# Performance work log

Measured on AMD Instinct MI355X. Metric: run time of the kernel, lower is better.

## Reference

```python
import jax, jax.numpy as jnp
import numpy as np

D_MODEL = 1024
N_HEAD = 16
HEAD_DIM = D_MODEL // N_HEAD  # 64
D_FF = 4096
BATCH = 4
SEQ = 2048
EPS = 1e-5
ROPE_BASE = 10000.0


def _xavier(key, shape):
    fan_in, fan_out = shape[1], shape[0]
    limit = np.sqrt(6.0 / (fan_in + fan_out))
    return jax.random.uniform(key, shape, jnp.float32, -limit, limit)


def setup_inputs() -> dict:
    key = jax.random.key(0)
    ks = jax.random.split(key, 8)
    return {
        "src": jax.random.normal(ks[0], (BATCH, SEQ, D_MODEL), jnp.float32),
        "Wqkv": _xavier(ks[1], (3 * D_MODEL, D_MODEL)),   # torch Linear weight layout [out,in]
        "Wout": _xavier(ks[2], (D_MODEL, D_MODEL)),
        "g1": jnp.ones((D_MODEL,), jnp.float32),           # RMSNorm weights
        "g2": jnp.ones((D_MODEL,), jnp.float32),
        "W1": _xavier(ks[3], (D_FF, D_MODEL)),              # GeGLU w1
        "W2": _xavier(ks[4], (D_MODEL, D_FF)),              # GeGLU w2
        "W3": _xavier(ks[5], (D_FF, D_MODEL)),              # GeGLU w3
    }


def _rmsnorm(x, g, eps=EPS):
    return x * jax.lax.rsqrt(jnp.mean(x * x, axis=-1, keepdims=True) + eps) * g


def _rope(x):
    # x: [B, H, S, head_dim], interleaved even/odd rotation (matches torch stack+flatten)
    seq = x.shape[-2]
    inv_freq = 1.0 / (ROPE_BASE ** (jnp.arange(0, HEAD_DIM, 2, dtype=jnp.float32) / HEAD_DIM))
    t = jnp.arange(seq, dtype=jnp.float32)
    freqs = t[:, None] * inv_freq[None, :]          # [S, head_dim/2]
    cos, sin = jnp.cos(freqs), jnp.sin(freqs)
    x = x.astype(jnp.float32)
    x_even = x[..., 0::2]
    x_odd = x[..., 1::2]
    rot_even = x_even * cos - x_odd * sin
    rot_odd = x_odd * cos + x_even * sin
    return jnp.stack([rot_even, rot_odd], axis=-1).reshape(x.shape)


def reference(src, Wqkv, Wout, g1, g2, W1, W2, W3):
    B, S, _ = src.shape
    # --- attention block (pre-norm) ---
    xn = _rmsnorm(src, g1)
    qkv = xn @ Wqkv.T                                        # [B,S,3*D]
    qkv = qkv.reshape(B, S, 3, N_HEAD, HEAD_DIM).transpose(2, 0, 3, 1, 4)  # [3,B,H,S,hd]
    q, k, v = qkv[0], qkv[1], qkv[2]
    q = _rope(q)
    k = _rope(k)
    scale = 1.0 / jnp.sqrt(jnp.float32(HEAD_DIM))
    scores = jnp.einsum("bhqd,bhkd->bhqk", q, k) * scale
    probs = jax.nn.softmax(scores, axis=-1)
    attn = jnp.einsum("bhqk,bhkd->bhqd", probs, v)           # [B,H,S,hd]
    attn = attn.transpose(0, 2, 1, 3).reshape(B, S, D_MODEL)
    x = src + attn @ Wout.T
    # --- GeGLU FFN block (pre-norm) ---
    xn2 = _rmsnorm(x, g2)
    ff = (jax.nn.gelu(xn2 @ W1.T, approximate=False) * (xn2 @ W3.T)) @ W2.T
    return x + ff
```

## Files before the change

kernel.cpp:

```cpp
#include <hip/hip_runtime.h>

#define DEVI __device__ __forceinline__

typedef __attribute__((ext_vector_type(8))) short s8v;
typedef __attribute__((ext_vector_type(4))) float f4v;

DEVI unsigned short f2bf(float f) {
  unsigned int u = __float_as_uint(f);
  return (unsigned short)((u + 0x7FFFu + ((u >> 16) & 1u)) >> 16);
}
DEVI float bf2f(unsigned short h) { return __uint_as_float(((unsigned int)h) << 16); }

DEVI f4v mfma16(s8v a, s8v b, f4v c) {
  asm("v_mfma_f32_16x16x32_bf16 %0, %1, %2, %0" : "+v"(c) : "v"(a), "v"(b));
  return c;
}

DEVI float fexp2(float x) {
  float r;
  asm("v_exp_f32 %0, %1" : "=v"(r) : "v"(x));
  return r;
}

DEVI unsigned int cvtpk_bf16(float lo, float hi) {
  unsigned int r;
  asm("v_cvt_pk_bf16_f32 %0, %1, %2" : "=v"(r) : "v"(lo), "v"(hi));
  return r;
}

DEVI float gelu_t(float x) {
  const float t = x * x;
  const float a = __builtin_fmaf(t, -0.10295555f, -2.30225854f);
  return x / (1.0f + fexp2(x * a));
}

DEVI void gload_lds16(const void* g, void* l) {
  __builtin_amdgcn_global_load_lds(
      (__attribute__((address_space(1))) void*)g,
      (__attribute__((address_space(3))) void*)l, 16, 0, 0);
}

DEVI void barrier_raw() {
  asm volatile("" ::: "memory");
  __builtin_amdgcn_s_barrier();
  asm volatile("" ::: "memory");
}

DEVI void map_block(int bid, int nbx, int gw, int& by, int& bx) {
  const int xcd = bid & 7;
  const int local = bid >> 3;
  const int grp = gw * 8;
  const int q = local / grp;
  const int rem = local - q * grp;
  by = xcd * 8 + (rem & 7);
  bx = q * gw + (rem >> 3);
}

__global__ __launch_bounds__(256)
void cvt_all_k(const float* __restrict__ Wqkv, const float* __restrict__ Wout,
               const float* __restrict__ W2, const float* __restrict__ W1,
               const float* __restrict__ W3,
               unsigned short* __restrict__ wQKV, unsigned short* __restrict__ wOut,
               unsigned short* __restrict__ wW2, unsigned short* __restrict__ wI) {
  const int i = blockIdx.x * 256 + threadIdx.x;
  const float4* src;
  ushort4* dst;
  if (i < 786432) {
    src = (const float4*)Wqkv + i;
    dst = (ushort4*)wQKV + i;
  } else if (i < 1048576) {
    const int j = i - 786432;
    src = (const float4*)Wout + j;
    dst = (ushort4*)wOut + j;
  } else if (i < 2097152) {
    const int j = i - 1048576;
    src = (const float4*)W2 + j;
    dst = (ushort4*)wW2 + j;
  } else {
    const int j = i - 2097152;
    const int g = j >> 8;
    const int c4 = j & 255;
    const int srow = ((g >> 7) << 6) + (g & 63);
    const float* s = ((g >> 6) & 1) ? W3 : W1;
    src = (const float4*)(s + (size_t)srow * 1024) + c4;
    dst = (ushort4*)(wI + (size_t)g * 1024) + c4;
  }
  const float4 v = *src;
  ushort4 ov;
  ov.x = f2bf(v.x); ov.y = f2bf(v.y); ov.z = f2bf(v.z); ov.w = f2bf(v.w);
  *dst = ov;
}

__global__ __launch_bounds__(256)
void rmsnorm_k(const float* __restrict__ x, const float* __restrict__ g,
               unsigned short* __restrict__ o) {
  const int row = blockIdx.x;
  const int tid = threadIdx.x;
  const float4 v = ((const float4*)(x + (size_t)row * 1024))[tid];
  float ss = v.x * v.x + v.y * v.y + v.z * v.z + v.w * v.w;
#pragma unroll
  for (int off = 32; off > 0; off >>= 1) ss += __shfl_down(ss, off);
  __shared__ float wsum[4];
  if ((tid & 63) == 0) wsum[tid >> 6] = ss;
  __syncthreads();
  const float tot = wsum[0] + wsum[1] + wsum[2] + wsum[3];
  const float sc = rsqrtf(tot * (1.0f / 1024.0f) + 1e-5f);
  const float4 gv = ((const float4*)g)[tid];
  ushort4 ov;
  ov.x = f2bf(v.x * sc * gv.x);
  ov.y = f2bf(v.y * sc * gv.y);
  ov.z = f2bf(v.z * sc * gv.z);
  ov.w = f2bf(v.w * sc * gv.w);
  ((ushort4*)(o + (size_t)row * 1024))[tid] = ov;
}

__global__ __launch_bounds__(256)
void rmsnorm_b(const unsigned short* __restrict__ x, const float* __restrict__ g,
               unsigned short* __restrict__ o) {
  const int row = blockIdx.x;
  const int tid = threadIdx.x;
  const ushort4 hv = ((const ushort4*)(x + (size_t)row * 1024))[tid];
  float v0 = bf2f(hv.x), v1 = bf2f(hv.y), v2 = bf2f(hv.z), v3 = bf2f(hv.w);
  float ss = v0 * v0 + v1 * v1 + v2 * v2 + v3 * v3;
#pragma unroll
  for (int off = 32; off > 0; off >>= 1) ss += __shfl_down(ss, off);
  __shared__ float wsum[4];
  if ((tid & 63) == 0) wsum[tid >> 6] = ss;
  __syncthreads();
  const float tot = wsum[0] + wsum[1] + wsum[2] + wsum[3];
  const float sc = rsqrtf(tot * (1.0f / 1024.0f) + 1e-5f);
  const float4 gv = ((const float4*)g)[tid];
  ushort4 ov;
  ov.x = f2bf(v0 * sc * gv.x);
  ov.y = f2bf(v1 * sc * gv.y);
  ov.z = f2bf(v2 * sc * gv.z);
  ov.w = f2bf(v3 * sc * gv.w);
  ((ushort4*)(o + (size_t)row * 1024))[tid] = ov;
}

__global__ __launch_bounds__(256)
void rope_table_k(float* __restrict__ cosT, float* __restrict__ sinT) {
  const int idx = blockIdx.x * 256 + threadIdx.x;
  const int s = idx >> 5, p = idx & 31;
  const float inv = powf(10000.0f, -(float)(2 * p) * (1.0f / 64.0f));
  const float a = (float)s * inv;
  cosT[idx] = cosf(a);
  sinT[idx] = sinf(a);
}

__global__ __launch_bounds__(256)
void vtrans_k(const unsigned short* __restrict__ v, unsigned short* __restrict__ vT) {
  __shared__ unsigned short t[64][72];
  const int bh = blockIdx.y;
  const int s0 = blockIdx.x * 64;
  const int tid = threadIdx.x;
  const int r = tid >> 3;
  const int c8 = (tid & 7) * 8;
  const unsigned short* src = v + ((size_t)bh * 2048 + s0) * 64;
#pragma unroll
  for (int it = 0; it < 2; ++it) {
    const int row = it * 32 + r;
    s8v d = *(const s8v*)(src + row * 64 + c8);
    *(s8v*)(&t[row][c8]) = d;
  }
  __syncthreads();
  unsigned short* dst = vT + (size_t)bh * 64 * 2048 + s0;
#pragma unroll
  for (int it = 0; it < 2; ++it) {
    const int d = it * 32 + r;
    s8v o;
#pragma unroll
    for (int m = 0; m < 8; ++m) o[m] = (short)t[c8 + m][d];
    *(s8v*)(dst + (size_t)d * 2048 + c8) = o;
  }
}

template <int EPI>
__global__ __launch_bounds__(256)
void gemm_bt(const unsigned short* __restrict__ A,
             const unsigned short* __restrict__ Bt,
             const int K, const int N, const int nbx, const int gw,
             unsigned short* Cb, float* Cf, const float* Xadd,
             unsigned short* __restrict__ Qp, unsigned short* __restrict__ Kp,
             unsigned short* __restrict__ Vp,
             const float* __restrict__ cosT, const float* __restrict__ sinT) {
  __shared__ __align__(16) unsigned char sA[128 * 128];
  __shared__ __align__(16) unsigned char sB[128 * 128];
  const int tid = threadIdx.x;
  const int lane = tid & 63;
  const int wave = tid >> 6;
  const int wr = (wave >> 1) * 64, wc = (wave & 1) * 64;
  int by, bx;
  map_block(blockIdx.x, nbx, gw, by, bx);
  const int row0 = by * 128;
  const int col0 = bx * 128;

  int ldsOff[4], gOffA[4], gOffB[4];
#pragma unroll
  for (int it = 0; it < 4; ++it) {
    const int p = it * 4096 + tid * 16;
    const int row = p >> 7;
    const int inner = (p & 127) ^ ((row & 7) << 4);
    ldsOff[it] = p;
    gOffA[it] = (row0 + row) * K + (inner >> 1);
    gOffB[it] = (col0 + row) * K + (inner >> 1);
  }

  f4v acc[4][4];
  const f4v fzero = {0.f, 0.f, 0.f, 0.f};
#pragma unroll
  for (int i = 0; i < 4; ++i)
#pragma unroll
    for (int j = 0; j < 4; ++j) acc[i][j] = fzero;

  const int cbase = (lane >> 4) * 16;
  const int rlane = lane & 15;

  for (int kt = 0; kt < K; kt += 64) {
    __syncthreads();
#pragma unroll
    for (int it = 0; it < 4; ++it) {
      gload_lds16(A + gOffA[it] + kt, sA + ldsOff[it]);
      gload_lds16(Bt + gOffB[it] + kt, sB + ldsOff[it]);
    }
    asm volatile("s_waitcnt vmcnt(0)" ::: "memory");
    __syncthreads();

#pragma unroll
    for (int ks = 0; ks < 2; ++ks) {
      const int cb = ks * 64 + cbase;
      s8v af[4], bfv[4];
#pragma unroll
      for (int i = 0; i < 4; ++i) {
        const int r = wr + i * 16 + rlane;
        af[i] = *(const s8v*)(sA + r * 128 + (cb ^ ((r & 7) << 4)));
      }
#pragma unroll
      for (int j = 0; j < 4; ++j) {
        const int r = wc + j * 16 + rlane;
        bfv[j] = *(const s8v*)(sB + r * 128 + (cb ^ ((r & 7) << 4)));
      }
#pragma unroll
      for (int i = 0; i < 4; ++i)
#pragma unroll
        for (int j = 0; j < 4; ++j) acc[i][j] = mfma16(af[i], bfv[j], acc[i][j]);
    }
  }

  const int rquad = (lane >> 4) * 4;

  if constexpr (EPI == 4) {
    __syncthreads();
    float* xbuf = (wave & 2) ? (float*)sB : (float*)sA;
    if (wave & 1) {
#pragma unroll
      for (int i = 0; i < 2; ++i)
#pragma unroll
        for (int j = 0; j < 4; ++j)
#pragma unroll
          for (int r = 0; r < 4; ++r)
            xbuf[((i * 16 + rquad + r) << 6) + j * 16 + rlane] = acc[i][j][r];
    } else {
#pragma unroll
      for (int i = 0; i < 2; ++i)
#pragma unroll
        for (int j = 0; j < 4; ++j)
#pragma unroll
          for (int r = 0; r < 4; ++r)
            xbuf[2048 + ((i * 16 + rquad + r) << 6) + j * 16 + rlane] = acc[2 + i][j][r];
    }
    __syncthreads();
    if (!(wave & 1)) {
#pragma unroll
      for (int i = 0; i < 2; ++i)
#pragma unroll
        for (int j = 0; j < 4; ++j)
#pragma unroll
          for (int r = 0; r < 4; ++r) {
            const int t = i * 16 + rquad + r;
            const float h1v = acc[i][j][r];
            const float h3v = xbuf[(t << 6) + j * 16 + rlane];
            Cb[(size_t)(row0 + wr + t) * N + (size_t)bx * 64 + j * 16 + rlane] =
                f2bf(gelu_t(h1v) * h3v);
          }
    } else {
#pragma unroll
      for (int i = 0; i < 2; ++i)
#pragma unroll
        for (int j = 0; j < 4; ++j)
#pragma unroll
          for (int r = 0; r < 4; ++r) {
            const int t = i * 16 + rquad + r;
            const float h1v = xbuf[2048 + (t << 6) + j * 16 + rlane];
            const float h3v = acc[2 + i][j][r];
            Cb[(size_t)(row0 + wr + 32 + t) * N + (size_t)bx * 64 + j * 16 + rlane] =
                f2bf(gelu_t(h1v) * h3v);
          }
    }
    return;
  }

#pragma unroll
  for (int i = 0; i < 4; ++i) {
#pragma unroll
    for (int j = 0; j < 4; ++j) {
#pragma unroll
      for (int r = 0; r < 4; ++r) {
        const int row = row0 + wr + i * 16 + rquad + r;
        const int col = col0 + wc + j * 16 + rlane;
        const float v = acc[i][j][r];
        if constexpr (EPI == 1) {
          const float partner = __shfl_xor(v, 1);
          const int which = col >> 10;
          const int rem = col & 1023;
          const int s = row & 2047;
          const int p = (rem & 63) >> 1;
          const float c = cosT[(s << 5) + p];
          const float sn = sinT[(s << 5) + p];
          const float sg = (rem & 1) ? sn : -sn;
          const float roped = __builtin_fmaf(partner, sg, v * c);
          const size_t idx =
              (((size_t)(row >> 11) * 16 + (rem >> 6)) * 2048 + (row & 2047)) * 64 + (rem & 63);
          if (which == 0) Qp[idx] = f2bf(roped * (0.125f * 1.44269504089f));
          else if (which == 1) Kp[idx] = f2bf(roped);
          else Vp[idx] = f2bf(v);
        } else if constexpr (EPI == 5) {
          const size_t idx = (size_t)row * N + col;
          Cb[idx] = f2bf(Xadd[idx] + v);
        } else {
          const size_t idx = (size_t)row * N + col;
          Cf[idx] = bf2f(Qp[idx]) + v;
        }
      }
    }
  }
}

__global__ __launch_bounds__(256)
void attn_k(const unsigned short* __restrict__ Qg,
            const unsigned short* __restrict__ Kg,
            const unsigned short* __restrict__ VTg,
            unsigned short* __restrict__ Og) {
  __shared__ __align__(16) unsigned char sK[2][8192];
  __shared__ __align__(16) unsigned char sV[2][8192];

  const int tid = threadIdx.x, lane = tid & 63, wave = tid >> 6;
  int id = blockIdx.x;
  id = (id & 7) * 128 + (id >> 3);
  const int qt = id & 15, h = (id >> 4) & 15, b = id >> 8;
  const size_t bh = (size_t)b * 16 + h;
  const unsigned short* qb = Qg + (bh * 2048 + (size_t)qt * 128 + wave * 32) * 64;
  const unsigned short* kbp = Kg + bh * 2048 * 64;
  const unsigned short* vb = VTg + bh * 64 * 2048;

  const int g = lane >> 4;
  const int rl = lane & 15;
  const int cbase = g * 16;

  s8v qf[2][2];
#pragma unroll
  for (int qs = 0; qs < 2; ++qs) {
    const unsigned short* qrow = qb + (size_t)(qs * 16 + rl) * 64 + g * 8;
    qf[qs][0] = *(const s8v*)(qrow);
    qf[qs][1] = *(const s8v*)(qrow + 32);
  }

  const f4v fzero = {0.f, 0.f, 0.f, 0.f};
  f4v of[2][4];
#pragma unroll
  for (int qs = 0; qs < 2; ++qs)
#pragma unroll
    for (int jd = 0; jd < 4; ++jd) of[qs][jd] = fzero;
  float l[2] = {0.f, 0.f};

  int ldsOff[2], koff[2], voff[2];
#pragma unroll
  for (int it = 0; it < 2; ++it) {
    const int p = it * 4096 + tid * 16;
    const int row = p >> 7;
    const int krow = (row & 32) | ((row & 12) << 1) | ((row & 16) >> 2) | (row & 3);
    const int inner = (p & 127) ^ ((row & 7) << 4);
    ldsOff[it] = p;
    koff[it] = krow * 64 + (inner >> 1);
    voff[it] = row * 2048 + (inner >> 1);
  }

#pragma unroll
  for (int it = 0; it < 2; ++it) {
    gload_lds16(kbp + koff[it], sK[0] + ldsOff[it]);
    gload_lds16(vb + voff[it], sV[0] + ldsOff[it]);
  }

  for (int t = 0; t < 32; ++t) {
    const int buf = t & 1;
    asm volatile("s_waitcnt vmcnt(0)" ::: "memory");
    barrier_raw();
    if (t < 31) {
      const size_t kt0 = (size_t)(t + 1) * 64;
#pragma unroll
      for (int it = 0; it < 2; ++it) {
        gload_lds16(kbp + kt0 * 64 + koff[it], sK[buf ^ 1] + ldsOff[it]);
        gload_lds16(vb + kt0 + voff[it], sV[buf ^ 1] + ldsOff[it]);
      }
    }

    f4v sc[2][4];
#pragma unroll
    for (int qs = 0; qs < 2; ++qs)
#pragma unroll
      for (int jk = 0; jk < 4; ++jk) sc[qs][jk] = fzero;
    __builtin_amdgcn_s_setprio(1);
#pragma unroll
    for (int ks = 0; ks < 2; ++ks) {
      const int cb = ks * 64 + cbase;
#pragma unroll
      for (int jk = 0; jk < 4; ++jk) {
        const int r = jk * 16 + rl;
        s8v kf = *(const s8v*)(sK[buf] + r * 128 + (cb ^ ((r & 7) << 4)));
        sc[0][jk] = mfma16(kf, qf[0][ks], sc[0][jk]);
        sc[1][jk] = mfma16(kf, qf[1][ks], sc[1][jk]);
      }
    }
    __builtin_amdgcn_s_setprio(0);

#pragma unroll
    for (int qs = 0; qs < 2; ++qs) {
      float rs = 0.f;
#pragma unroll
      for (int jk = 0; jk < 4; ++jk)
#pragma unroll
        for (int mm = 0; mm < 4; ++mm) {
          const float p = fexp2(sc[qs][jk][mm]);
          sc[qs][jk][mm] = p;
          rs += p;
        }
      l[qs] += rs;
    }

    s8v pa[2][2];
#pragma unroll
    for (int qs = 0; qs < 2; ++qs) {
#pragma unroll
      for (int ks = 0; ks < 2; ++ks) {
        union { s8v v; unsigned int u[4]; } pk;
        pk.u[0] = cvtpk_bf16(sc[qs][2 * ks][0], sc[qs][2 * ks][1]);
        pk.u[1] = cvtpk_bf16(sc[qs][2 * ks][2], sc[qs][2 * ks][3]);
        pk.u[2] = cvtpk_bf16(sc[qs][2 * ks + 1][0], sc[qs][2 * ks + 1][1]);
        pk.u[3] = cvtpk_bf16(sc[qs][2 * ks + 1][2], sc[qs][2 * ks + 1][3]);
        pa[qs][ks] = pk.v;
      }
    }

    __builtin_amdgcn_s_setprio(1);
#pragma unroll
    for (int ks = 0; ks < 2; ++ks) {
      const int cb = ks * 64 + cbase;
#pragma unroll
      for (int jd = 0; jd < 4; ++jd) {
        const int r = jd * 16 + rl;
        s8v vf = *(const s8v*)(sV[buf] + r * 128 + (cb ^ ((r & 7) << 4)));
        of[0][jd] = mfma16(pa[0][ks], vf, of[0][jd]);
        of[1][jd] = mfma16(pa[1][ks], vf, of[1][jd]);
      }
    }
    __builtin_amdgcn_s_setprio(0);
  }

#pragma unroll
  for (int qs = 0; qs < 2; ++qs) {
    float lt = l[qs];
    lt += __shfl_xor(lt, 16);
    lt += __shfl_xor(lt, 32);
    const float inv = 1.0f / lt;
#pragma unroll
    for (int r = 0; r < 4; ++r) {
      const float ivr = __shfl(inv, g * 20 + r);
      const int qrow = qt * 128 + wave * 32 + qs * 16 + g * 4 + r;
      const size_t obase = ((size_t)b * 2048 + qrow) * 1024 + h * 64;
#pragma unroll
      for (int jd = 0; jd < 4; ++jd) Og[obase + jd * 16 + rl] = f2bf(of[qs][jd][r] * ivr);
    }
  }
}

extern "C" void kernel_launch(void* const* d_in, const int* in_sizes, int n_in,
                              void* d_out, int out_size, void* d_ws, size_t ws_size,
                              hipStream_t stream) {
  (void)in_sizes; (void)n_in; (void)out_size; (void)ws_size;
  const float* src  = (const float*)d_in[0];
  const float* Wqkv = (const float*)d_in[1];
  const float* Wout = (const float*)d_in[2];
  const float* g1   = (const float*)d_in[3];
  const float* g2   = (const float*)d_in[4];
  const float* W1   = (const float*)d_in[5];
  const float* W2   = (const float*)d_in[6];
  const float* W3   = (const float*)d_in[7];
  float* out = (float*)d_out;

  char* ws = (char*)d_ws;
  size_t off = 0;
  auto take = [&](size_t bytes) -> char* {
    char* p = ws + off;
    off += (bytes + 255) & ~(size_t)255;
    return p;
  };
  unsigned short* wQKV = (unsigned short*)take((size_t)3072 * 1024 * 2);
  unsigned short* wOut = (unsigned short*)take((size_t)1024 * 1024 * 2);
  unsigned short* wI   = (unsigned short*)take((size_t)8192 * 1024 * 2);
  unsigned short* wW2  = (unsigned short*)take((size_t)1024 * 4096 * 2);
  unsigned short* xn   = (unsigned short*)take((size_t)8192 * 1024 * 2);
  unsigned short* q    = (unsigned short*)take((size_t)64 * 2048 * 64 * 2);
  unsigned short* kb   = (unsigned short*)take((size_t)64 * 2048 * 64 * 2);
  unsigned short* v    = (unsigned short*)take((size_t)64 * 2048 * 64 * 2);
  unsigned short* vT   = (unsigned short*)take((size_t)64 * 64 * 2048 * 2);
  float* cosT = (float*)take((size_t)2048 * 32 * 4);
  float* sinT = (float*)take((size_t)2048 * 32 * 4);
  unsigned short* h1   = (unsigned short*)take((size_t)8192 * 4096 * 2);

  cvt_all_k<<<dim3(16384), dim3(256), 0, stream>>>(Wqkv, Wout, W2, W1, W3,
                                                   wQKV, wOut, wW2, wI);
  rope_table_k<<<dim3(2048 * 32 / 256), dim3(256), 0, stream>>>(cosT, sinT);

  rmsnorm_k<<<dim3(8192), dim3(256), 0, stream>>>(src, g1, xn);
  gemm_bt<1><<<dim3(1536), dim3(256), 0, stream>>>(xn, wQKV, 1024, 3072, 24, 8,
                                                   nullptr, nullptr, nullptr, q, kb, v, cosT, sinT);
  vtrans_k<<<dim3(32, 64), dim3(256), 0, stream>>>(v, vT);
  attn_k<<<dim3(1024), dim3(256), 0, stream>>>(q, kb, vT, xn);
  gemm_bt<5><<<dim3(512), dim3(256), 0, stream>>>(xn, wOut, 1024, 1024, 8, 4,
                                                  q, nullptr, src, nullptr, nullptr, nullptr,
                                                  nullptr, nullptr);
  rmsnorm_b<<<dim3(8192), dim3(256), 0, stream>>>(q, g2, xn);
  gemm_bt<4><<<dim3(4096), dim3(256), 0, stream>>>(xn, wI, 1024, 4096, 64, 8,
                                                   h1, nullptr, nullptr, nullptr, nullptr, nullptr,
                                                   nullptr, nullptr);
  gemm_bt<6><<<dim3(512), dim3(256), 0, stream>>>(h1, wW2, 4096, 1024, 8, 2,
                                                  nullptr, out, nullptr, q, nullptr, nullptr,
                                                  nullptr, nullptr);
}
```

Measured before the change: 438.0 us.

## Fuse V transpose into QKV GEMM epilogue and swizzle GeGLU LDS exchange

The QKV GEMM epilogue now handles V column blocks separately: it stages the tile in shared memory and writes V already transposed into the vT layout. This removes the separate vtrans kernel and the round trip of V through global memory. The GeGLU epilogue's LDS exchange buffer gets an XOR swizzle to reduce bank conflicts. In exchange, V blocks pay extra syncs and LDS traffic inside the GEMM.

```diff
diff --git a/kernel.cpp b/kernel.cpp
--- a/kernel.cpp
+++ b/kernel.cpp
@@ -148,33 +148,6 @@
   sinT[idx] = sinf(a);
 }
 
-__global__ __launch_bounds__(256)
-void vtrans_k(const unsigned short* __restrict__ v, unsigned short* __restrict__ vT) {
-  __shared__ unsigned short t[64][72];
-  const int bh = blockIdx.y;
-  const int s0 = blockIdx.x * 64;
-  const int tid = threadIdx.x;
-  const int r = tid >> 3;
-  const int c8 = (tid & 7) * 8;
-  const unsigned short* src = v + ((size_t)bh * 2048 + s0) * 64;
-#pragma unroll
-  for (int it = 0; it < 2; ++it) {
-    const int row = it * 32 + r;
-    s8v d = *(const s8v*)(src + row * 64 + c8);
-    *(s8v*)(&t[row][c8]) = d;
-  }
-  __syncthreads();
-  unsigned short* dst = vT + (size_t)bh * 64 * 2048 + s0;
-#pragma unroll
-  for (int it = 0; it < 2; ++it) {
-    const int d = it * 32 + r;
-    s8v o;
-#pragma unroll
-    for (int m = 0; m < 8; ++m) o[m] = (short)t[c8 + m][d];
-    *(s8v*)(dst + (size_t)d * 2048 + c8) = o;
-  }
-}
-
 template <int EPI>
 __global__ __launch_bounds__(256)
 void gemm_bt(const unsigned short* __restrict__ A,
@@ -184,8 +157,9 @@
              unsigned short* __restrict__ Qp, unsigned short* __restrict__ Kp,
              unsigned short* __restrict__ Vp,
              const float* __restrict__ cosT, const float* __restrict__ sinT) {
-  __shared__ __align__(16) unsigned char sA[128 * 128];
-  __shared__ __align__(16) unsigned char sB[128 * 128];
+  __shared__ __align__(16) unsigned char smem[32768];
+  unsigned char* sA = smem;
+  unsigned char* sB = smem + 16384;
   const int tid = threadIdx.x;
   const int lane = tid & 63;
   const int wave = tid >> 6;
@@ -258,16 +232,22 @@
 #pragma unroll
         for (int j = 0; j < 4; ++j)
 #pragma unroll
-          for (int r = 0; r < 4; ++r)
-            xbuf[((i * 16 + rquad + r) << 6) + j * 16 + rlane] = acc[i][j][r];
+          for (int r = 0; r < 4; ++r) {
+            const int t = i * 16 + rquad + r;
+            const int cs = (j * 16 + rlane) ^ (((t >> 2) & 1) << 4);
+            xbuf[(t << 6) + cs] = acc[i][j][r];
+          }
     } else {
 #pragma unroll
       for (int i = 0; i < 2; ++i)
 #pragma unroll
         for (int j = 0; j < 4; ++j)
 #pragma unroll
-          for (int r = 0; r < 4; ++r)
-            xbuf[2048 + ((i * 16 + rquad + r) << 6) + j * 16 + rlane] = acc[2 + i][j][r];
+          for (int r = 0; r < 4; ++r) {
+            const int t = i * 16 + rquad + r;
+            const int cs = (j * 16 + rlane) ^ (((t >> 2) & 1) << 4);
+            xbuf[2048 + (t << 6) + cs] = acc[2 + i][j][r];
+          }
     }
     __syncthreads();
     if (!(wave & 1)) {
@@ -278,8 +258,9 @@
 #pragma unroll
           for (int r = 0; r < 4; ++r) {
             const int t = i * 16 + rquad + r;
+            const int cs = (j * 16 + rlane) ^ (((t >> 2) & 1) << 4);
             const float h1v = acc[i][j][r];
-            const float h3v = xbuf[(t << 6) + j * 16 + rlane];
+            const float h3v = xbuf[(t << 6) + cs];
             Cb[(size_t)(row0 + wr + t) * N + (size_t)bx * 64 + j * 16 + rlane] =
                 f2bf(gelu_t(h1v) * h3v);
           }
@@ -291,7 +272,8 @@
 #pragma unroll
           for (int r = 0; r < 4; ++r) {
             const int t = i * 16 + rquad + r;
-            const float h1v = xbuf[2048 + (t << 6) + j * 16 + rlane];
+            const int cs = (j * 16 + rlane) ^ (((t >> 2) & 1) << 4);
+            const float h1v = xbuf[2048 + (t << 6) + cs];
             const float h3v = acc[2 + i][j][r];
             Cb[(size_t)(row0 + wr + 32 + t) * N + (size_t)bx * 64 + j * 16 + rlane] =
                 f2bf(gelu_t(h1v) * h3v);
@@ -300,16 +282,45 @@
     return;
   }
 
-#pragma unroll
-  for (int i = 0; i < 4; ++i) {
-#pragma unroll
-    for (int j = 0; j < 4; ++j) {
-#pragma unroll
-      for (int r = 0; r < 4; ++r) {
-        const int row = row0 + wr + i * 16 + rquad + r;
-        const int col = col0 + wc + j * 16 + rlane;
-        const float v = acc[i][j][r];
-        if constexpr (EPI == 1) {
+  if constexpr (EPI == 1) {
+    if (bx >= 16) {
+      __syncthreads();
+#pragma unroll
+      for (int i = 0; i < 4; ++i) {
+#pragma unroll
+        for (int j = 0; j < 4; ++j) {
+#pragma unroll
+          for (int rp = 0; rp < 4; rp += 2) {
+            const int c = wc + j * 16 + rlane;
+            const int s = wr + i * 16 + rquad + rp;
+            const unsigned int u = cvtpk_bf16(acc[i][j][rp], acc[i][j][rp + 1]);
+            *(unsigned int*)(smem + c * 256 + ((2 * s) ^ ((c & 7) << 4))) = u;
+          }
+        }
+      }
+      __syncthreads();
+      const int b = row0 >> 11, s0 = row0 & 2047;
+      const int hbase = (bx - 16) * 2;
+#pragma unroll
+      for (int t8 = 0; t8 < 8; ++t8) {
+        const int gidx = t8 * 256 + tid;
+        const int c = gidx >> 4, ch = gidx & 15;
+        s8v val = *(const s8v*)(smem + c * 256 + ((ch * 16) ^ ((c & 7) << 4)));
+        const int bh = b * 16 + hbase + (c >> 6);
+        const int d = c & 63;
+        *(s8v*)(Vp + ((size_t)bh * 64 + d) * 2048 + s0 + ch * 8) = val;
+      }
+      return;
+    }
+#pragma unroll
+    for (int i = 0; i < 4; ++i) {
+#pragma unroll
+      for (int j = 0; j < 4; ++j) {
+#pragma unroll
+        for (int r = 0; r < 4; ++r) {
+          const int row = row0 + wr + i * 16 + rquad + r;
+          const int col = col0 + wc + j * 16 + rlane;
+          const float v = acc[i][j][r];
           const float partner = __shfl_xor(v, 1);
           const int which = col >> 10;
           const int rem = col & 1023;
@@ -322,12 +333,26 @@
           const size_t idx =
               (((size_t)(row >> 11) * 16 + (rem >> 6)) * 2048 + (row & 2047)) * 64 + (rem & 63);
           if (which == 0) Qp[idx] = f2bf(roped * (0.125f * 1.44269504089f));
-          else if (which == 1) Kp[idx] = f2bf(roped);
-          else Vp[idx] = f2bf(v);
-        } else if constexpr (EPI == 5) {
+          else Kp[idx] = f2bf(roped);
+        }
+      }
+    }
+    return;
+  }
+
+#pragma unroll
+  for (int i = 0; i < 4; ++i) {
+#pragma unroll
+    for (int j = 0; j < 4; ++j) {
+#pragma unroll
+      for (int r = 0; r < 4; ++r) {
+        const int row = row0 + wr + i * 16 + rquad + r;
+        const int col = col0 + wc + j * 16 + rlane;
+        const float v = acc[i][j][r];
+        if constexpr (EPI == 5) {
           const size_t idx = (size_t)row * N + col;
           Cb[idx] = f2bf(Xadd[idx] + v);
-        } else {
+        } else if constexpr (EPI == 6) {
           const size_t idx = (size_t)row * N + col;
           Cf[idx] = bf2f(Qp[idx]) + v;
         }
@@ -511,7 +536,6 @@
   unsigned short* xn   = (unsigned short*)take((size_t)8192 * 1024 * 2);
   unsigned short* q    = (unsigned short*)take((size_t)64 * 2048 * 64 * 2);
   unsigned short* kb   = (unsigned short*)take((size_t)64 * 2048 * 64 * 2);
-  unsigned short* v    = (unsigned short*)take((size_t)64 * 2048 * 64 * 2);
   unsigned short* vT   = (unsigned short*)take((size_t)64 * 64 * 2048 * 2);
   float* cosT = (float*)take((size_t)2048 * 32 * 4);
   float* sinT = (float*)take((size_t)2048 * 32 * 4);
@@ -523,8 +547,7 @@
 
   rmsnorm_k<<<dim3(8192), dim3(256), 0, stream>>>(src, g1, xn);
   gemm_bt<1><<<dim3(1536), dim3(256), 0, stream>>>(xn, wQKV, 1024, 3072, 24, 8,
-                                                   nullptr, nullptr, nullptr, q, kb, v, cosT, sinT);
-  vtrans_k<<<dim3(32, 64), dim3(256), 0, stream>>>(v, vT);
+                                                   nullptr, nullptr, nullptr, q, kb, vT, cosT, sinT);
   attn_k<<<dim3(1024), dim3(256), 0, stream>>>(q, kb, vT, xn);
   gemm_bt<5><<<dim3(512), dim3(256), 0, stream>>>(xn, wOut, 1024, 1024, 8, 4,
                                                   q, nullptr, src, nullptr, nullptr, nullptr,
```

After: 416.2 us. 1.05x faster.
